# Optimization experiments

Measured on AMD Instinct MI355X. Metric: run time of the kernel, lower is better.

The kernel has to match this reference:

```python
import jax, jax.numpy as jnp
import numpy as np

N, K, D = 524288, 32, 64


def setup_inputs() -> dict:
    key = jax.random.key(0)
    k1, k2 = jax.random.split(key)
    X = jax.random.normal(k1, (N, D), dtype=jnp.float32)
    mu = jax.random.uniform(k2, (K, D), dtype=jnp.float32)
    var = jnp.ones((K, D), dtype=jnp.float32)
    pi = jnp.ones((K, 1), dtype=jnp.float32) / K  # uniform mixture weights, as in __init__
    return {"X": X, "mu": mu, "var": var, "pi": pi}


def reference(X, mu, var, pi):
    # One EM iteration (the body of GaussianMixture.fit).
    n = X.shape[0]
    log2pi = jnp.log(jnp.asarray(2.0 * np.pi, dtype=X.dtype))
    inv_var = 1.0 / var  # (K, D)
    # log_pk[k, n] = sum_d log N(x_nd; mu_kd, var_kd), via quadratic expansion
    # (same math as the broadcast (K, N, D) tensor, without materializing it).
    quad = (
        jnp.einsum("kd,nd->kn", inv_var, X * X)
        - 2.0 * jnp.einsum("kd,nd->kn", mu * inv_var, X)
        + jnp.sum(mu * mu * inv_var, axis=-1, keepdims=True)
    )  # (K, N)
    log_det = jnp.sum(jnp.log(var) + log2pi, axis=-1, keepdims=True)  # (K, 1)
    log_pk = -0.5 * (quad + log_det)  # (K, N)
    # E-step: responsibilities via stable logsumexp over components
    log_post = jnp.log(pi) + log_pk  # (K, N)
    log_norm = jax.scipy.special.logsumexp(log_post, axis=0, keepdims=True)
    r = jnp.exp(log_post - log_norm)  # (K, N)
    # M-step
    dem = jnp.sum(r, axis=1, keepdims=True)  # (K, 1)
    pi_new = dem / n
    rx = r @ X            # (K, D)
    rx2 = r @ (X * X)     # (K, D)
    mu_new = rx / dem
    # sum_n r_kn (x_nd - mu_new_kd)^2 = rx2 - 2 mu_new * rx + mu_new^2 * dem
    var_new = (rx2 - 2.0 * mu_new * rx + mu_new * mu_new * dem) / dem
    return jnp.concatenate([pi_new, mu_new, var_new], axis=1)  # (K, 1 + 2D)
```

## Files before the change

### kernel.cpp

```cpp
#include <hip/hip_runtime.h>
#include <hip/hip_bf16.h>
#include <math.h>
#include <string.h>

#define NPTS 524288
#define KC 32
#define DIM 64
#define NTILES 4096
#define PROW 4128
#define GRIDX 512

typedef __attribute__((ext_vector_type(8)))  short short8v;
typedef __attribute__((ext_vector_type(16))) float f32x16;

#define RL_BASE  32768
#define WL_BASE  40960
#define CL_BASE  49152
#define SMEM_BYTES 49280

__device__ __forceinline__ unsigned short s2bf(float a) {
    __hip_bfloat16 h = __float2bfloat16(a);
    unsigned short u;
    memcpy(&u, &h, 2);
    return u;
}
__device__ __forceinline__ unsigned pk2bf(float a, float b) {
    return (unsigned)s2bf(a) | ((unsigned)s2bf(b) << 16);
}

__device__ __forceinline__ void stage_chunk(unsigned char* xt, int w, int c, float4 v, int l) {
    int pt   = w * 32 + c * 4 + (l >> 4);
    int colB = (l & 15) * 8;
    int swz  = (pt & 15) << 4;
    uint2 bx, bx2;
    bx.x  = pk2bf(v.x, v.y);              bx.y  = pk2bf(v.z, v.w);
    bx2.x = pk2bf(v.x * v.x, v.y * v.y);  bx2.y = pk2bf(v.z * v.z, v.w * v.w);
    *(uint2*)(xt + pt * 256 + (colB ^ swz))         = bx;
    *(uint2*)(xt + pt * 256 + ((128 + colB) ^ swz)) = bx2;
}

__global__ __launch_bounds__(256, 2)
void gmm_main(const float* __restrict__ X, const float* __restrict__ mu,
              const float* __restrict__ var, const float* __restrict__ pi,
              float* __restrict__ partials, int g) {
    __shared__ unsigned char smem[SMEM_BYTES];

    const int tid = threadIdx.x;
    const int l   = tid & 63;
    const int w   = tid >> 6;
    const int lm  = l & 31;
    const int lh  = l >> 5;
    const int mypt = w * 32 + lm;

    const float4* X4 = (const float4*)X;

    float4 xr[8];
    {
        const float4* xs = X4 + (size_t)blockIdx.x * 2048 + w * 512;
#pragma unroll
        for (int c = 0; c < 8; ++c) xr[c] = xs[c * 64 + l];
    }

    {
        int comp = tid >> 3, i8 = tid & 7;
        unsigned char* wrow = smem + WL_BASE + comp * 256;
        int swz = (comp & 15) << 4;
        if (i8 < 4) {
            int d0 = i8 * 16;
            const float* mm = mu  + comp * DIM + d0;
            const float* vv = var + comp * DIM + d0;
#pragma unroll
            for (int j = 0; j < 8; ++j) {
                unsigned u = pk2bf(mm[2*j] / vv[2*j], mm[2*j+1] / vv[2*j+1]);
                int k = d0 + 2 * j;
                *(unsigned*)(wrow + ((k * 2) ^ swz)) = u;
            }
        } else {
            int d0 = (i8 - 4) * 16;
            const float* vv = var + comp * DIM + d0;
#pragma unroll
            for (int j = 0; j < 8; ++j) {
                unsigned u = pk2bf(-0.5f / vv[2*j], -0.5f / vv[2*j+1]);
                int k = 64 + d0 + 2 * j;
                *(unsigned*)(wrow + ((k * 2) ^ swz)) = u;
            }
        }
        float* clp = (float*)smem;
        const float* vv = var + comp * DIM + i8 * 8;
        const float* mm = mu  + comp * DIM + i8 * 8;
        float p = 0.0f;
#pragma unroll
        for (int j = 0; j < 8; ++j) { float v = vv[j], m2 = mm[j]; p += m2 * m2 / v + logf(v); }
        clp[tid] = p;
    }
    __syncthreads();
    if (tid < KC) {
        float* clp = (float*)smem;
        float ssum = 0.0f;
#pragma unroll
        for (int j = 0; j < 8; ++j) ssum += clp[tid * 8 + j];
        const float LOG2PI = 1.8378770664093453f;
        ((float*)(smem + CL_BASE))[tid] = logf(pi[tid]) - 0.5f * (ssum + DIM * LOG2PI);
    }
    __syncthreads();

    const float* cl = (const float*)(smem + CL_BASE);

    short8v onesf;
#pragma unroll
    for (int j = 0; j < 8; ++j) onesf[j] = (short)0x3F80;

    f32x16 rxacc, demA;
#pragma unroll
    for (int i = 0; i < 16; ++i) { rxacc[i] = 0.0f; demA[i] = 0.0f; }

    for (int tile = blockIdx.x; tile < NTILES; tile += g) {
#pragma unroll
        for (int c = 0; c < 8; ++c) stage_chunk(smem, w, c, xr[c], l);

        if (tile + g < NTILES) {
            const float4* xs = X4 + (size_t)(tile + g) * 2048 + w * 512;
#pragma unroll
            for (int c = 0; c < 8; ++c) xr[c] = xs[c * 64 + l];
        }

        f32x16 s;
#pragma unroll
        for (int r = 0; r < 16; ++r) s[r] = 0.0f;
#pragma unroll
        for (int ks = 0; ks < 8; ++ks) {
            short8v a = *(const short8v*)(smem + WL_BASE + lm * 256 +
                                          ((ks * 32 + lh * 16) ^ ((lm & 15) << 4)));
            short8v b = *(const short8v*)(smem + mypt * 256 +
                                          ((ks * 32 + lh * 16) ^ ((lm & 15) << 4)));
            s = __builtin_amdgcn_mfma_f32_32x32x16_bf16(a, b, s, 0, 0, 0);
        }

#pragma unroll
        for (int r = 0; r < 16; ++r) s[r] += cl[(r & 3) + 8 * (r >> 2) + 4 * lh];
        float m = s[0];
#pragma unroll
        for (int r = 1; r < 16; ++r) m = fmaxf(m, s[r]);
        m = fmaxf(m, __shfl_xor(m, 32, 64));
        float sum = 0.0f;
#pragma unroll
        for (int r = 0; r < 16; ++r) { s[r] = __expf(s[r] - m); sum += s[r]; }
        sum += __shfl_xor(sum, 32, 64);
        float inv = 1.0f / sum;
#pragma unroll
        for (int r = 0; r < 16; ++r) {
            float rv = s[r] * inv;
            int comp = (r & 3) + 8 * (r >> 2) + 4 * lh;
            *(unsigned short*)(smem + RL_BASE + comp * 256 +
                               ((mypt * 2) ^ ((comp & 15) << 4))) = s2bf(rv);
        }

        asm volatile("s_waitcnt lgkmcnt(0)" ::: "memory");
        __builtin_amdgcn_s_barrier();
        __builtin_amdgcn_sched_barrier(0);

#pragma unroll
        for (int ks = 0; ks < 8; ++ks) {
            short8v af = *(const short8v*)(smem + RL_BASE + lm * 256 +
                                           ((ks * 32 + lh * 16) ^ ((lm & 15) << 4)));
            short8v bv;
#pragma unroll
            for (int j = 0; j < 8; ++j) {
                int pt = ks * 16 + lh * 8 + j;
                bv[j] = *(const short*)(smem + pt * 256 +
                                        ((mypt * 2) ^ ((pt & 15) << 4)));
            }
            rxacc = __builtin_amdgcn_mfma_f32_32x32x16_bf16(af, bv, rxacc, 0, 0, 0);
            demA  = __builtin_amdgcn_mfma_f32_32x32x16_bf16(af, onesf, demA, 0, 0, 0);
        }
        __syncthreads();
    }

    float* P = partials + (size_t)blockIdx.x * PROW;
#pragma unroll
    for (int r = 0; r < 16; ++r) {
        int comp = (r & 3) + 8 * (r >> 2) + 4 * lh;
        P[32 + comp * 128 + w * 32 + lm] = rxacc[r];
    }
    if (w == 0 && lm == 0) {
#pragma unroll
        for (int r = 0; r < 16; ++r)
            P[(r & 3) + 8 * (r >> 2) + 4 * lh] = demA[r];
    }
}

__global__ __launch_bounds__(512)
void gmm_reduce(const float* __restrict__ partials, float* __restrict__ out, int nb) {
    __shared__ float red[512 * 4];
    __shared__ float dred[512];
    __shared__ float rxf[128];
    const int k = blockIdx.x;
    const int t = threadIdx.x;
    const int f4i   = t & 31;
    const int chunk = t >> 5;

    float4 s4 = {0.f, 0.f, 0.f, 0.f};
    const int R = nb >> 4;
#pragma unroll 4
    for (int j = 0; j < R; ++j) {
        int b = chunk * R + j;
        float4 v = *((const float4*)(partials + (size_t)b * PROW + 32 + k * 128) + f4i);
        s4.x += v.x; s4.y += v.y; s4.z += v.z; s4.w += v.w;
    }
    float dp = 0.0f;
    for (int b = t; b < nb; b += 512) dp += partials[(size_t)b * PROW + k];

    *(float4*)(red + t * 4) = s4;
    dred[t] = dp;
    __syncthreads();
    for (int off = 256; off >= 1; off >>= 1) {
        if (t < off) dred[t] += dred[t + off];
        __syncthreads();
    }
    if (t < 32) {
        float4 a = {0.f, 0.f, 0.f, 0.f};
#pragma unroll
        for (int c = 0; c < 16; ++c) {
            float4 v = *(const float4*)(red + (c * 32 + t) * 4);
            a.x += v.x; a.y += v.y; a.z += v.z; a.w += v.w;
        }
        *(float4*)(rxf + t * 4) = a;
    }
    __syncthreads();
    float dem = dred[0];
    if (t < 64) {
        float inv = 1.0f / dem;
        float rx  = rxf[t];
        float rx2 = rxf[t + 64];
        float muv = rx * inv;
        float va  = rx2 * inv - muv * muv;
        out[k * 129 + 1 + t]  = muv;
        out[k * 129 + 65 + t] = va;
        if (t == 0) out[k * 129] = dem * (1.0f / (float)NPTS);
    }
}

extern "C" void kernel_launch(void* const* d_in, const int* in_sizes, int n_in,
                              void* d_out, int out_size, void* d_ws, size_t ws_size,
                              hipStream_t stream) {
    const float* X   = (const float*)d_in[0];
    const float* mu  = (const float*)d_in[1];
    const float* var = (const float*)d_in[2];
    const float* pi  = (const float*)d_in[3];

    float* partials = (float*)d_ws;
    float* out      = (float*)d_out;

    int g = GRIDX;
    while (g > 64 && (size_t)g * PROW * 4 > ws_size) g >>= 1;

    gmm_main<<<g, 256, 0, stream>>>(X, mu, var, pi, partials, g);
    gmm_reduce<<<KC, 512, 0, stream>>>(partials, out, g);
}
```

Before: 40.46 us.

## Double-buffer LDS tiles, store only X and square in registers

Staging now writes only bf16 X (128 bytes per point) and computes X² in registers from the bf16 values, for both the log-likelihood MFMA and the M-step. Two X tiles and two responsibility buffers alternate so the trailing __syncthreads per tile can be dropped. The max and sum reductions are also tree-shaped. This halves LDS staging writes and removes one barrier per tile, at the cost of extra VALU squaring. Squaring an already-rounded bf16 value adds a second rounding step, which changes numerics slightly.

```diff
diff --git a/kernel.cpp b/kernel.cpp
--- a/kernel.cpp
+++ b/kernel.cpp
@@ -13,10 +13,12 @@
 typedef __attribute__((ext_vector_type(8)))  short short8v;
 typedef __attribute__((ext_vector_type(16))) float f32x16;
 
-#define RL_BASE  32768
-#define WL_BASE  40960
-#define CL_BASE  49152
-#define SMEM_BYTES 49280
+#define XT_SZ    16384
+#define RL0      32768
+#define RL_SZ    8192
+#define WL_BASE  49152
+#define CL_BASE  57344
+#define SMEM_BYTES 57472
 
 __device__ __forceinline__ unsigned short s2bf(float a) {
     __hip_bfloat16 h = __float2bfloat16(a);
@@ -28,15 +30,25 @@
     return (unsigned)s2bf(a) | ((unsigned)s2bf(b) << 16);
 }
 
+__device__ __forceinline__ short8v sq_bf16x8(short8v a) {
+    union { short8v s; unsigned u[4]; } in, out;
+    in.s = a;
+#pragma unroll
+    for (int i = 0; i < 4; ++i) {
+        float lo = __uint_as_float(in.u[i] << 16);
+        float hi = __uint_as_float(in.u[i] & 0xffff0000u);
+        out.u[i] = pk2bf(lo * lo, hi * hi);
+    }
+    return out.s;
+}
+
 __device__ __forceinline__ void stage_chunk(unsigned char* xt, int w, int c, float4 v, int l) {
     int pt   = w * 32 + c * 4 + (l >> 4);
     int colB = (l & 15) * 8;
-    int swz  = (pt & 15) << 4;
-    uint2 bx, bx2;
-    bx.x  = pk2bf(v.x, v.y);              bx.y  = pk2bf(v.z, v.w);
-    bx2.x = pk2bf(v.x * v.x, v.y * v.y);  bx2.y = pk2bf(v.z * v.z, v.w * v.w);
-    *(uint2*)(xt + pt * 256 + (colB ^ swz))         = bx;
-    *(uint2*)(xt + pt * 256 + ((128 + colB) ^ swz)) = bx2;
+    int swz  = (pt & 7) << 4;
+    uint2 bx;
+    bx.x = pk2bf(v.x, v.y);  bx.y = pk2bf(v.z, v.w);
+    *(uint2*)(xt + pt * 128 + (colB ^ swz)) = bx;
 }
 
 __global__ __launch_bounds__(256, 2)
@@ -114,9 +126,13 @@
 #pragma unroll
     for (int i = 0; i < 16; ++i) { rxacc[i] = 0.0f; demA[i] = 0.0f; }
 
+    int bufsel = 0;
     for (int tile = blockIdx.x; tile < NTILES; tile += g) {
-#pragma unroll
-        for (int c = 0; c < 8; ++c) stage_chunk(smem, w, c, xr[c], l);
+        unsigned char* xt = smem + bufsel * XT_SZ;
+        unsigned char* rl = smem + RL0 + bufsel * RL_SZ;
+
+#pragma unroll
+        for (int c = 0; c < 8; ++c) stage_chunk(xt, w, c, xr[c], l);
 
         if (tile + g < NTILES) {
             const float4* xs = X4 + (size_t)(tile + g) * 2048 + w * 512;
@@ -127,31 +143,44 @@
         f32x16 s;
 #pragma unroll
         for (int r = 0; r < 16; ++r) s[r] = 0.0f;
-#pragma unroll
-        for (int ks = 0; ks < 8; ++ks) {
+        short8v bf[4];
+#pragma unroll
+        for (int ks = 0; ks < 4; ++ks) {
             short8v a = *(const short8v*)(smem + WL_BASE + lm * 256 +
                                           ((ks * 32 + lh * 16) ^ ((lm & 15) << 4)));
-            short8v b = *(const short8v*)(smem + mypt * 256 +
+            bf[ks] = *(const short8v*)(xt + mypt * 128 +
+                                       ((ks * 32 + lh * 16) ^ ((mypt & 7) << 4)));
+            s = __builtin_amdgcn_mfma_f32_32x32x16_bf16(a, bf[ks], s, 0, 0, 0);
+        }
+#pragma unroll
+        for (int ks = 4; ks < 8; ++ks) {
+            short8v a = *(const short8v*)(smem + WL_BASE + lm * 256 +
                                           ((ks * 32 + lh * 16) ^ ((lm & 15) << 4)));
-            s = __builtin_amdgcn_mfma_f32_32x32x16_bf16(a, b, s, 0, 0, 0);
+            s = __builtin_amdgcn_mfma_f32_32x32x16_bf16(a, sq_bf16x8(bf[ks - 4]), s, 0, 0, 0);
         }
 
 #pragma unroll
         for (int r = 0; r < 16; ++r) s[r] += cl[(r & 3) + 8 * (r >> 2) + 4 * lh];
-        float m = s[0];
-#pragma unroll
-        for (int r = 1; r < 16; ++r) m = fmaxf(m, s[r]);
-        m = fmaxf(m, __shfl_xor(m, 32, 64));
-        float sum = 0.0f;
-#pragma unroll
-        for (int r = 0; r < 16; ++r) { s[r] = __expf(s[r] - m); sum += s[r]; }
+        float m0 = fmaxf(fmaxf(s[0],  s[1]),  fmaxf(s[2],  s[3]));
+        float m1 = fmaxf(fmaxf(s[4],  s[5]),  fmaxf(s[6],  s[7]));
+        float m2 = fmaxf(fmaxf(s[8],  s[9]),  fmaxf(s[10], s[11]));
+        float m3 = fmaxf(fmaxf(s[12], s[13]), fmaxf(s[14], s[15]));
+        float mx = fmaxf(fmaxf(m0, m1), fmaxf(m2, m3));
+        mx = fmaxf(mx, __shfl_xor(mx, 32, 64));
+#pragma unroll
+        for (int r = 0; r < 16; ++r) s[r] = __expf(s[r] - mx);
+        float s0 = (s[0] + s[1]) + (s[2] + s[3]);
+        float s1 = (s[4] + s[5]) + (s[6] + s[7]);
+        float s2 = (s[8] + s[9]) + (s[10] + s[11]);
+        float s3 = (s[12] + s[13]) + (s[14] + s[15]);
+        float sum = (s0 + s1) + (s2 + s3);
         sum += __shfl_xor(sum, 32, 64);
         float inv = 1.0f / sum;
 #pragma unroll
         for (int r = 0; r < 16; ++r) {
             float rv = s[r] * inv;
             int comp = (r & 3) + 8 * (r >> 2) + 4 * lh;
-            *(unsigned short*)(smem + RL_BASE + comp * 256 +
+            *(unsigned short*)(rl + comp * 256 +
                                ((mypt * 2) ^ ((comp & 15) << 4))) = s2bf(rv);
         }
 
@@ -161,19 +190,20 @@
 
 #pragma unroll
         for (int ks = 0; ks < 8; ++ks) {
-            short8v af = *(const short8v*)(smem + RL_BASE + lm * 256 +
+            short8v af = *(const short8v*)(rl + lm * 256 +
                                            ((ks * 32 + lh * 16) ^ ((lm & 15) << 4)));
             short8v bv;
+            int cb = (mypt & 63) * 2;
 #pragma unroll
             for (int j = 0; j < 8; ++j) {
                 int pt = ks * 16 + lh * 8 + j;
-                bv[j] = *(const short*)(smem + pt * 256 +
-                                        ((mypt * 2) ^ ((pt & 15) << 4)));
+                bv[j] = *(const short*)(xt + pt * 128 + (cb ^ ((pt & 7) << 4)));
             }
+            if (w >= 2) bv = sq_bf16x8(bv);
             rxacc = __builtin_amdgcn_mfma_f32_32x32x16_bf16(af, bv, rxacc, 0, 0, 0);
             demA  = __builtin_amdgcn_mfma_f32_32x32x16_bf16(af, onesf, demA, 0, 0, 0);
         }
-        __syncthreads();
+        bufsel ^= 1;
     }
 
     float* P = partials + (size_t)blockIdx.x * PROW;
```

Result: slower. 42.58 us (+5.2%).

## Replace per-block partials and reduce kernel with global atomics plus finalize

Applied to the files above, without the earlier changes.

Each block now atomically adds its rx/rx2 and responsibility-sum accumulators into one small global buffer, which is zeroed by a memset first. This replaces writing a full partials row per block and reducing them in a separate 32-block kernel. A tiny finalize kernel then computes pi, mu and var. This removes the partials traffic and the heavier reduction pass, but adds a memset launch, atomic contention across 512 blocks on about 4K addresses, and summation order that is no longer deterministic.

```diff
diff --git a/kernel.cpp b/kernel.cpp
--- a/kernel.cpp
+++ b/kernel.cpp
@@ -7,8 +7,8 @@
 #define KC 32
 #define DIM 64
 #define NTILES 4096
-#define PROW 4128
 #define GRIDX 512
+#define ACC_FLOATS (KC + KC * 128)
 
 typedef __attribute__((ext_vector_type(8)))  short short8v;
 typedef __attribute__((ext_vector_type(16))) float f32x16;
@@ -42,7 +42,7 @@
 __global__ __launch_bounds__(256, 2)
 void gmm_main(const float* __restrict__ X, const float* __restrict__ mu,
               const float* __restrict__ var, const float* __restrict__ pi,
-              float* __restrict__ partials, int g) {
+              float* __restrict__ acc, int g) {
     __shared__ unsigned char smem[SMEM_BYTES];
 
     const int tid = threadIdx.x;
@@ -176,68 +176,32 @@
         __syncthreads();
     }
 
-    float* P = partials + (size_t)blockIdx.x * PROW;
 #pragma unroll
     for (int r = 0; r < 16; ++r) {
         int comp = (r & 3) + 8 * (r >> 2) + 4 * lh;
-        P[32 + comp * 128 + w * 32 + lm] = rxacc[r];
+        atomicAdd(&acc[KC + comp * 128 + w * 32 + lm], rxacc[r]);
     }
     if (w == 0 && lm == 0) {
 #pragma unroll
         for (int r = 0; r < 16; ++r)
-            P[(r & 3) + 8 * (r >> 2) + 4 * lh] = demA[r];
-    }
-}
-
-__global__ __launch_bounds__(512)
-void gmm_reduce(const float* __restrict__ partials, float* __restrict__ out, int nb) {
-    __shared__ float red[512 * 4];
-    __shared__ float dred[512];
-    __shared__ float rxf[128];
-    const int k = blockIdx.x;
-    const int t = threadIdx.x;
-    const int f4i   = t & 31;
-    const int chunk = t >> 5;
-
-    float4 s4 = {0.f, 0.f, 0.f, 0.f};
-    const int R = nb >> 4;
-#pragma unroll 4
-    for (int j = 0; j < R; ++j) {
-        int b = chunk * R + j;
-        float4 v = *((const float4*)(partials + (size_t)b * PROW + 32 + k * 128) + f4i);
-        s4.x += v.x; s4.y += v.y; s4.z += v.z; s4.w += v.w;
-    }
-    float dp = 0.0f;
-    for (int b = t; b < nb; b += 512) dp += partials[(size_t)b * PROW + k];
-
-    *(float4*)(red + t * 4) = s4;
-    dred[t] = dp;
-    __syncthreads();
-    for (int off = 256; off >= 1; off >>= 1) {
-        if (t < off) dred[t] += dred[t + off];
-        __syncthreads();
-    }
-    if (t < 32) {
-        float4 a = {0.f, 0.f, 0.f, 0.f};
-#pragma unroll
-        for (int c = 0; c < 16; ++c) {
-            float4 v = *(const float4*)(red + (c * 32 + t) * 4);
-            a.x += v.x; a.y += v.y; a.z += v.z; a.w += v.w;
-        }
-        *(float4*)(rxf + t * 4) = a;
-    }
-    __syncthreads();
-    float dem = dred[0];
-    if (t < 64) {
-        float inv = 1.0f / dem;
-        float rx  = rxf[t];
-        float rx2 = rxf[t + 64];
-        float muv = rx * inv;
-        float va  = rx2 * inv - muv * muv;
-        out[k * 129 + 1 + t]  = muv;
-        out[k * 129 + 65 + t] = va;
-        if (t == 0) out[k * 129] = dem * (1.0f / (float)NPTS);
-    }
+            atomicAdd(&acc[(r & 3) + 8 * (r >> 2) + 4 * lh], demA[r]);
+    }
+}
+
+__global__ __launch_bounds__(256)
+void gmm_finalize(const float* __restrict__ acc, float* __restrict__ out) {
+    int t = threadIdx.x + blockIdx.x * blockDim.x;
+    if (t >= KC * DIM) return;
+    int k = t >> 6, d = t & 63;
+    float dm  = acc[k];
+    float iv  = 1.0f / dm;
+    float rx  = acc[KC + k * 128 + d];
+    float rx2 = acc[KC + k * 128 + 64 + d];
+    float muv = rx * iv;
+    float vav = rx2 * iv - muv * muv;
+    out[k * 129 + 1 + d]  = muv;
+    out[k * 129 + 65 + d] = vav;
+    if (d == 0) out[k * 129] = dm * (1.0f / (float)NPTS);
 }
 
 extern "C" void kernel_launch(void* const* d_in, const int* in_sizes, int n_in,
@@ -248,12 +212,10 @@
     const float* var = (const float*)d_in[2];
     const float* pi  = (const float*)d_in[3];
 
-    float* partials = (float*)d_ws;
-    float* out      = (float*)d_out;
-
-    int g = GRIDX;
-    while (g > 64 && (size_t)g * PROW * 4 > ws_size) g >>= 1;
-
-    gmm_main<<<g, 256, 0, stream>>>(X, mu, var, pi, partials, g);
-    gmm_reduce<<<KC, 512, 0, stream>>>(partials, out, g);
-}
+    float* acc = (float*)d_ws;
+    float* out = (float*)d_out;
+
+    (void)hipMemsetAsync(acc, 0, ACC_FLOATS * sizeof(float), stream);
+    gmm_main<<<GRIDX, 256, 0, stream>>>(X, mu, var, pi, acc, GRIDX);
+    gmm_finalize<<<8, 256, 0, stream>>>(acc, out);
+}
```

Result: slower. 94.41 us (+133.3%).
